# Kernel optimization log

Measured on AMD Instinct MI355X. Metric: run time of the kernel, lower is better.

The kernel has to match this reference:

```python
import jax, jax.numpy as jnp
import numpy as np

C = 128        # in_channels
HEADS = 4
B, D, H, W = 4, 16, 64, 64  # H must equal W for this module's matmul to type-check


def conv1x1(x, Wm, b):
    # 1x1x1 Conv3d == per-voxel linear over channels
    return jnp.einsum('bcdhw,oc->bodhw', x, Wm) + b[None, :, None, None, None]


def setup_inputs() -> dict:
    key = jax.random.key(0)
    ks = jax.random.split(key, 14)
    scale = 1.0 / np.sqrt(C)

    def wmat(k):
        return jax.random.normal(k, (C, C), jnp.float32) * scale

    def bvec(k):
        return jax.random.normal(k, (C,), jnp.float32) * 0.01

    return {
        'x':  jax.random.normal(ks[0], (B, C, D, H, W), jnp.float32),
        'Wq': wmat(ks[1]),  'bq': bvec(ks[2]),
        'Wk': wmat(ks[3]),  'bk': bvec(ks[4]),
        'Wv': wmat(ks[5]),  'bv': bvec(ks[6]),
        'Wa1': wmat(ks[7]), 'ba1': bvec(ks[8]),
        'Wa2': wmat(ks[9]), 'ba2': bvec(ks[10]),
        'Wf': wmat(ks[11]), 'bf': bvec(ks[12]),
    }


def reference(x, Wq, bq, Wk, bk, Wv, bv, Wa1, ba1, Wa2, ba2, Wf, bf):
    b, c, d, h, w = x.shape
    ch = c // HEADS  # channels per head

    q = conv1x1(x, Wq, bq).reshape(b, HEADS, ch, d, h, w)
    k = conv1x1(x, Wk, bk).reshape(b, HEADS, ch, d, h, w)
    v = conv1x1(x, Wv, bv).reshape(b, HEADS, ch, d, h, w)

    # attention over the last spatial axis: (W, H)^T @ (H, W) -> (W, W)
    attn = jnp.einsum('bhcdxi,bhcdxj->bhcdij', q, k)  # [b, heads, ch, d, W, W]
    attn = jax.nn.softmax(attn, axis=-1)
    # (W, W) @ (H=W, W) -> (W, W)
    out = jnp.einsum('bhcdik,bhcdkj->bhcdij', attn, v)
    out = out.reshape(b, c, d, h, w)

    # depth=1 attention layer: conv1x1 -> relu -> conv1x1
    out = conv1x1(jax.nn.relu(conv1x1(out, Wa1, ba1)), Wa2, ba2)
    out = conv1x1(out, Wf, bf)
    return out
```

## Files before the change

kernel.cpp:

```cpp
#include <hip/hip_runtime.h>


#define CCH 128
#define SPB 65536
#define NBATCH 4
#define WTAB 16384

typedef float f32x4 __attribute__((ext_vector_type(4)));
typedef __bf16 bf16x8 __attribute__((ext_vector_type(8)));
typedef short s16x8 __attribute__((ext_vector_type(8)));
typedef unsigned short u16x8 __attribute__((ext_vector_type(8)));
typedef unsigned short u16x4 __attribute__((ext_vector_type(4)));
typedef unsigned int u32x2 __attribute__((ext_vector_type(2)));

template <typename T>
static __device__ __forceinline__ auto mfma_try(T a, T b, f32x4 c, int)
    -> decltype(__builtin_amdgcn_mfma_f32_16x16x32_bf16(a, b, c, 0, 0, 0)) {
  return __builtin_amdgcn_mfma_f32_16x16x32_bf16(a, b, c, 0, 0, 0);
}
template <typename T>
static __device__ __forceinline__ f32x4 mfma_try(T a, T b, f32x4 c, long) {
  return __builtin_amdgcn_mfma_f32_16x16x32_bf16(
      __builtin_bit_cast(bf16x8, a), __builtin_bit_cast(bf16x8, b), c, 0, 0, 0);
}
static __device__ __forceinline__ f32x4 MFMA16(u16x8 a, u16x8 b, f32x4 c) {
  return mfma_try(__builtin_bit_cast(s16x8, a), __builtin_bit_cast(s16x8, b), c, 0);
}

static __device__ __forceinline__ unsigned short f2b(float f) {
  return __builtin_bit_cast(unsigned short, (__bf16)f);
}
static __device__ __forceinline__ unsigned int pk2(float a, float b) {
  return (unsigned int)f2b(a) | ((unsigned int)f2b(b) << 16);
}

static __device__ __forceinline__ void glds16(const unsigned short* g,
                                              unsigned short* l) {
  __builtin_amdgcn_global_load_lds(
      (const __attribute__((address_space(1))) unsigned int*)g,
      (__attribute__((address_space(3))) unsigned int*)l, 16, 0, 0);
}

static __device__ __forceinline__ void bar_lgkm() {
  asm volatile("s_waitcnt lgkmcnt(0)" ::: "memory");
  __builtin_amdgcn_sched_barrier(0);
  __builtin_amdgcn_s_barrier();
  __builtin_amdgcn_sched_barrier(0);
}
static __device__ __forceinline__ void bar_vm0() {
  asm volatile("s_waitcnt vmcnt(0)" ::: "memory");
  __builtin_amdgcn_sched_barrier(0);
  __builtin_amdgcn_s_barrier();
  __builtin_amdgcn_sched_barrier(0);
}

static __device__ __forceinline__ int swzc(int r, int c) {
  int slot = ((c >> 3) ^ (r & 7) ^ ((r >> 3) & 15)) & 15;
  return r * 128 + slot * 8 + (c & 7);
}
static __device__ __forceinline__ int widx(int r, int c) {
  return (r & 64) * 128 + swzc(r & 63, c);
}
static __device__ __forceinline__ int cbix(int o, int s) {
  int slot = ((s >> 3) ^ (o & 15)) & 15;
  return o * 128 + slot * 8 + (s & 7);
}
static __device__ __forceinline__ int swat(int w, int x) {
  int slot = ((x >> 3) ^ (w & 7) ^ ((w >> 3) & 7)) & 7;
  return w * 64 + slot * 8 + (x & 7);
}
static __device__ __forceinline__ int pix(int i, int j) {
  int slot = ((j >> 3) ^ (((i >> 2) & 3) << 1)) & 7;
  return i * 64 + slot * 8 + (j & 7);
}

__global__ __launch_bounds__(256) void prep_w_kernel(
    const float* __restrict__ Wq, const float* __restrict__ Wk,
    const float* __restrict__ Wv, const float* __restrict__ W1,
    const float* __restrict__ W2, const float* __restrict__ W3,
    unsigned short* __restrict__ out)
{
  const float* Ws[6] = {Wq, Wk, Wv, W1, W2, W3};
  const float* W = Ws[blockIdx.x];
  unsigned short* o = out + (size_t)blockIdx.x * WTAB;
  const int tid = threadIdx.x;
#pragma unroll
  for (int p = 0; p < 16; ++p) {
    const int base = p * 1024 + tid * 4;
    const int m = base >> 7;
    const int c0 = base & 127;
    f32x4 v = *(const f32x4*)&W[base];
    u16x4 u;
#pragma unroll
    for (int e = 0; e < 4; ++e) u[e] = f2b(v[e]);
    *(u16x4*)&o[widx(m, c0)] = u;
  }
}

__global__ __launch_bounds__(512, 2) void qkv_kernel(
    const float* __restrict__ X, const unsigned short* __restrict__ Wbf,
    const float* __restrict__ Bq, const float* __restrict__ Bk,
    const float* __restrict__ Bv,
    unsigned short* __restrict__ Yq, unsigned short* __restrict__ Yk,
    unsigned short* __restrict__ Yv)
{
  __shared__ unsigned short wt[3 * WTAB];
  __shared__ unsigned short xb[WTAB];

  const int tid  = threadIdx.x;
  const int wv   = tid >> 6;
  const int lane = tid & 63;
  const int lr   = lane & 15;
  const int lg   = lane >> 4;
  const int sbase = blockIdx.x * 512;
  const size_t xoff = (size_t)blockIdx.y * CCH * SPB;

  const int go = tid * 8;
#pragma unroll
  for (int t = 0; t < 3; ++t)
#pragma unroll
    for (int p = 0; p < 4; ++p)
      glds16(&Wbf[t * WTAB + p * 4096 + go], &wt[t * WTAB + p * 4096 + go]);

  float bq_v[8], bk_v[8], bv_v[8];
#pragma unroll
  for (int of = 0; of < 8; ++of) {
    bq_v[of] = Bq[of * 16 + lr];
    bk_v[of] = Bk[of * 16 + lr];
    bv_v[of] = Bv[of * 16 + lr];
  }

  const int c0  = (tid >> 3) * 2;
  const int sb8 = (tid & 7) * 4;
  const float* xrow = X + xoff + (size_t)c0 * SPB + sbase;
  unsigned int* xb32 = (unsigned int*)xb;

  f32x4 xr[8];
#pragma unroll
  for (int i = 0; i < 4; ++i) {
    xr[i]     = *(const f32x4*)&xrow[sb8 + 32 * i];
    xr[4 + i] = *(const f32x4*)&xrow[SPB + sb8 + 32 * i];
  }
#pragma unroll
  for (int i = 0; i < 4; ++i)
#pragma unroll
    for (int e = 0; e < 4; ++e)
      xb32[swzc(sb8 + 32 * i + e, c0) >> 1] = pk2(xr[i][e], xr[4 + i][e]);
  __syncthreads();

#pragma unroll
  for (int si = 0; si < 4; ++si) {
    const int sg = sbase + si * 128;

    u16x8 afr[4];
#pragma unroll
    for (int ks = 0; ks < 4; ++ks)
      afr[ks] = *(const u16x8*)&xb[swzc(wv * 16 + lr, ks * 32 + lg * 8)];

    if (si < 3) {
      const float* xn = xrow + (si + 1) * 128;
#pragma unroll
      for (int i = 0; i < 4; ++i) {
        xr[i]     = *(const f32x4*)&xn[sb8 + 32 * i];
        xr[4 + i] = *(const f32x4*)&xn[SPB + sb8 + 32 * i];
      }
    }
    bar_lgkm();

    auto conv = [&](int t, const float (&b8)[8], unsigned short* __restrict__ Y) {
      f32x4 acc[8];
#pragma unroll
      for (int of = 0; of < 8; ++of) {
        f32x4 z = {0.f, 0.f, 0.f, 0.f};
        acc[of] = z;
      }
#pragma unroll
      for (int ks = 0; ks < 4; ++ks) {
        const int k0 = ks * 32 + lg * 8;
#pragma unroll
        for (int of = 0; of < 8; ++of) {
          u16x8 wfr = *(const u16x8*)&wt[t * WTAB + widx(of * 16 + lr, k0)];
          acc[of] = MFMA16(afr[ks], wfr, acc[of]);
        }
      }
#pragma unroll
      for (int of = 0; of < 8; ++of) {
        const float b = b8[of];
        u32x2 pk;
        pk.x = pk2(acc[of][0] + b, acc[of][1] + b);
        pk.y = pk2(acc[of][2] + b, acc[of][3] + b);
        *(u32x2*)&xb[cbix(of * 16 + lr, wv * 16 + lg * 4)] = pk;
      }
      bar_lgkm();
#pragma unroll
      for (int p = 0; p < 4; ++p) {
        const int row = p * 32 + (tid >> 4);
        const int sc  = (tid & 15) * 8;
        u16x8 v = *(const u16x8*)&xb[cbix(row, sc)];
        *(u16x8*)&Y[xoff + (size_t)row * SPB + sg + sc] = v;
      }
      bar_lgkm();
    };

    conv(0, bq_v, Yq);
    conv(1, bk_v, Yk);
    conv(2, bv_v, Yv);

    if (si < 3) {
#pragma unroll
      for (int i = 0; i < 4; ++i)
#pragma unroll
        for (int e = 0; e < 4; ++e)
          xb32[swzc(sb8 + 32 * i + e, c0) >> 1] = pk2(xr[i][e], xr[4 + i][e]);
      __syncthreads();
    }
  }
}

__global__ __launch_bounds__(256, 4) void attn64_kernel(
    const unsigned short* __restrict__ Q,
    const unsigned short* __restrict__ K,
    const unsigned short* __restrict__ V,
    unsigned short* __restrict__ O)
{
  __shared__ unsigned short qt[4096];
  __shared__ unsigned short kt[4096];
  __shared__ unsigned short vt[4096];
  __shared__ unsigned short pbuf[4096];

  const int tid  = threadIdx.x;
  const int wv   = tid >> 6;
  const int lane = tid & 63;
  const int lr   = lane & 15;
  const int lg   = lane >> 4;
  const size_t base = (size_t)blockIdx.x * 4096;

  {
    const int x0 = (tid >> 3) * 2;
    const int w0 = (tid & 7) * 8;
    const size_t ga = base + (size_t)x0 * 64 + w0;
    u16x8 qa = *(const u16x8*)&Q[ga], qb = *(const u16x8*)&Q[ga + 64];
    u16x8 ka = *(const u16x8*)&K[ga], kb = *(const u16x8*)&K[ga + 64];
    u16x8 va = *(const u16x8*)&V[ga], vb = *(const u16x8*)&V[ga + 64];
    unsigned int* qt32 = (unsigned int*)qt;
    unsigned int* kt32 = (unsigned int*)kt;
    unsigned int* vt32 = (unsigned int*)vt;
#pragma unroll
    for (int e = 0; e < 8; ++e) {
      const int idx = swat(w0 + e, x0) >> 1;
      qt32[idx] = (unsigned int)qa[e] | ((unsigned int)qb[e] << 16);
      kt32[idx] = (unsigned int)ka[e] | ((unsigned int)kb[e] << 16);
      vt32[idx] = (unsigned int)va[e] | ((unsigned int)vb[e] << 16);
    }
  }
  __syncthreads();

  f32x4 sacc[4];
#pragma unroll
  for (int nf = 0; nf < 4; ++nf) { f32x4 z = {0.f, 0.f, 0.f, 0.f}; sacc[nf] = z; }
#pragma unroll
  for (int ks = 0; ks < 2; ++ks) {
    const int k0 = ks * 32 + lg * 8;
    u16x8 a = *(const u16x8*)&qt[swat(wv * 16 + lr, k0)];
#pragma unroll
    for (int nf = 0; nf < 4; ++nf) {
      u16x8 bb = *(const u16x8*)&kt[swat(nf * 16 + lr, k0)];
      sacc[nf] = MFMA16(a, bb, sacc[nf]);
    }
  }

#pragma unroll
  for (int r = 0; r < 4; ++r) {
    float m = fmaxf(fmaxf(sacc[0][r], sacc[1][r]), fmaxf(sacc[2][r], sacc[3][r]));
    m = fmaxf(m, __shfl_xor(m, 1));
    m = fmaxf(m, __shfl_xor(m, 2));
    m = fmaxf(m, __shfl_xor(m, 4));
    m = fmaxf(m, __shfl_xor(m, 8));
    float sum = 0.f;
#pragma unroll
    for (int nf = 0; nf < 4; ++nf) {
      float p = __expf(sacc[nf][r] - m);
      sacc[nf][r] = p;
      sum += p;
    }
    sum += __shfl_xor(sum, 1);
    sum += __shfl_xor(sum, 2);
    sum += __shfl_xor(sum, 4);
    sum += __shfl_xor(sum, 8);
    const float inv = 1.f / sum;
    const int i = wv * 16 + lg * 4 + r;
#pragma unroll
    for (int nf = 0; nf < 4; ++nf)
      pbuf[pix(i, nf * 16 + lr)] = f2b(sacc[nf][r] * inv);
  }

  f32x4 oacc[4];
#pragma unroll
  for (int nf = 0; nf < 4; ++nf) { f32x4 z = {0.f, 0.f, 0.f, 0.f}; oacc[nf] = z; }
#pragma unroll
  for (int ks = 0; ks < 2; ++ks) {
    const int k0 = ks * 32 + lg * 8;
    u16x8 a = *(const u16x8*)&pbuf[pix(wv * 16 + lr, k0)];
#pragma unroll
    for (int nf = 0; nf < 4; ++nf) {
      u16x8 bb = *(const u16x8*)&vt[swat(nf * 16 + lr, k0)];
      oacc[nf] = MFMA16(bb, a, oacc[nf]);
    }
  }

  {
    const size_t ib = base + (size_t)(16 * wv + lr) * 64 + lg * 4;
#pragma unroll
    for (int nf = 0; nf < 4; ++nf) {
      u32x2 pk;
      pk.x = pk2(oacc[nf][0], oacc[nf][1]);
      pk.y = pk2(oacc[nf][2], oacc[nf][3]);
      *(u32x2*)&O[ib + nf * 16] = pk;
    }
  }
}

__global__ __launch_bounds__(256, 2) void tail_kernel(
    const unsigned short* __restrict__ Xb, const unsigned short* __restrict__ Wbf,
    const float* __restrict__ B1, const float* __restrict__ B2,
    const float* __restrict__ B3, float* __restrict__ OUT)
{
  __shared__ unsigned short wl[16384];
  __shared__ unsigned short xc[16384];
  __shared__ float bias_lds[3][128];

  const int tid  = threadIdx.x;
  const int wv   = tid >> 6;
  const int lane = tid & 63;
  const int lr   = lane & 15;
  const int lg   = lane >> 4;
  const int s0   = blockIdx.x * 128;
  const size_t xbase = (size_t)blockIdx.y * CCH * SPB;
  const int go = tid * 8;

#pragma unroll
  for (int p = 0; p < 8; ++p) glds16(&Wbf[p * 2048 + go], &wl[p * 2048 + go]);

  if (tid < 128) {
    bias_lds[0][tid] = B1[tid];
    bias_lds[1][tid] = B2[tid];
    bias_lds[2][tid] = B3[tid];
  }

  {
    const int cp = tid >> 2;
    const int sq = tid & 3;
    const unsigned short* xa = Xb + xbase + (size_t)(2 * cp) * SPB + s0 + sq * 32;
    const unsigned short* xb = xa + SPB;
    unsigned int* xc32 = (unsigned int*)xc;
#pragma unroll
    for (int i = 0; i < 4; ++i) {
      u16x8 a = *(const u16x8*)&xa[8 * i];
      u16x8 b = *(const u16x8*)&xb[8 * i];
#pragma unroll
      for (int e = 0; e < 8; ++e)
        xc32[swzc(sq * 32 + 8 * i + e, 2 * cp) >> 1] =
            (unsigned int)a[e] | ((unsigned int)b[e] << 16);
    }
  }
  __syncthreads();

  u16x8 bfr[2][4];
#pragma unroll
  for (int nf = 0; nf < 2; ++nf)
#pragma unroll
    for (int ks = 0; ks < 4; ++ks)
      bfr[nf][ks] = *(const u16x8*)&xc[swzc(wv * 32 + nf * 16 + lr, ks * 32 + lg * 8)];

  f32x4 acc[8][2];
  auto gemm_std = [&]() {
#pragma unroll
    for (int mf = 0; mf < 8; ++mf)
#pragma unroll
      for (int nf = 0; nf < 2; ++nf) {
        f32x4 z = {0.f, 0.f, 0.f, 0.f};
        acc[mf][nf] = z;
      }
#pragma unroll
    for (int ks = 0; ks < 4; ++ks) {
      const int k0 = ks * 32 + lg * 8;
#pragma unroll
      for (int mf = 0; mf < 8; ++mf) {
        u16x8 afr = *(const u16x8*)&wl[widx(mf * 16 + lr, k0)];
        acc[mf][0] = MFMA16(afr, bfr[0][ks], acc[mf][0]);
        acc[mf][1] = MFMA16(afr, bfr[1][ks], acc[mf][1]);
      }
    }
  };

  auto epi_chain = [&](int ci, bool relu) {
#pragma unroll
    for (int mf = 0; mf < 8; ++mf)
#pragma unroll
      for (int nf = 0; nf < 2; ++nf) {
        const int s = wv * 32 + nf * 16 + lr;
        const int c0 = mf * 16 + lg * 4;
        f32x4 bb = *(const f32x4*)&bias_lds[ci][c0];
        float v0 = acc[mf][nf][0] + bb[0];
        float v1 = acc[mf][nf][1] + bb[1];
        float v2 = acc[mf][nf][2] + bb[2];
        float v3 = acc[mf][nf][3] + bb[3];
        if (relu) {
          v0 = fmaxf(v0, 0.f); v1 = fmaxf(v1, 0.f);
          v2 = fmaxf(v2, 0.f); v3 = fmaxf(v3, 0.f);
        }
        u32x2 pk;
        pk.x = pk2(v0, v1);
        pk.y = pk2(v2, v3);
        *(u32x2*)&xc[swzc(s, c0)] = pk;
      }
#pragma unroll
    for (int nf = 0; nf < 2; ++nf)
#pragma unroll
      for (int ks = 0; ks < 4; ++ks)
        bfr[nf][ks] = *(const u16x8*)&xc[swzc(wv * 32 + nf * 16 + lr, ks * 32 + lg * 8)];
  };

#pragma unroll
  for (int j = 0; j < 2; ++j) {
    gemm_std();
    bar_lgkm();
    const unsigned short* Wn = Wbf + (size_t)(j + 1) * WTAB;
#pragma unroll
    for (int p = 0; p < 8; ++p) glds16(&Wn[p * 2048 + go], &wl[p * 2048 + go]);
    epi_chain(j, j == 0);
    bar_vm0();
  }

  {
    f32x4 acc3[2][8];
#pragma unroll
    for (int sf = 0; sf < 2; ++sf)
#pragma unroll
      for (int of = 0; of < 8; ++of) {
        f32x4 z = {0.f, 0.f, 0.f, 0.f};
        acc3[sf][of] = z;
      }
#pragma unroll
    for (int ks = 0; ks < 4; ++ks) {
      const int k0 = ks * 32 + lg * 8;
#pragma unroll
      for (int of = 0; of < 8; ++of) {
        u16x8 wfr = *(const u16x8*)&wl[widx(of * 16 + lr, k0)];
        acc3[0][of] = MFMA16(bfr[0][ks], wfr, acc3[0][of]);
        acc3[1][of] = MFMA16(bfr[1][ks], wfr, acc3[1][of]);
      }
    }
    const int sb = s0 + wv * 32 + lg * 4;
#pragma unroll
    for (int sf = 0; sf < 2; ++sf)
#pragma unroll
      for (int of = 0; of < 8; ++of) {
        const float b = bias_lds[2][of * 16 + lr];
        f32x4 v = acc3[sf][of];
        v[0] += b; v[1] += b; v[2] += b; v[3] += b;
        *(f32x4*)&OUT[xbase + (size_t)(of * 16 + lr) * SPB + sb + sf * 16] = v;
      }
  }
}

extern "C" void kernel_launch(void* const* d_in, const int* in_sizes, int n_in,
                              void* d_out, int out_size, void* d_ws, size_t ws_size,
                              hipStream_t stream) {
  const float* x   = (const float*)d_in[0];
  const float* Wq  = (const float*)d_in[1];  const float* bq  = (const float*)d_in[2];
  const float* Wk  = (const float*)d_in[3];  const float* bk  = (const float*)d_in[4];
  const float* Wv  = (const float*)d_in[5];  const float* bv  = (const float*)d_in[6];
  const float* Wa1 = (const float*)d_in[7];  const float* ba1 = (const float*)d_in[8];
  const float* Wa2 = (const float*)d_in[9];  const float* ba2 = (const float*)d_in[10];
  const float* Wf  = (const float*)d_in[11]; const float* bf_ = (const float*)d_in[12];

  unsigned short* qb  = (unsigned short*)d_ws;
  unsigned short* wbf = qb + (size_t)NBATCH * CCH * SPB;
  unsigned short* kb = (unsigned short*)d_out;
  unsigned short* vb = kb + (size_t)NBATCH * CCH * SPB;

  prep_w_kernel<<<6, 256, 0, stream>>>(Wq, Wk, Wv, Wa1, Wa2, Wf, wbf);

  qkv_kernel<<<dim3(SPB / 512, NBATCH), 512, 0, stream>>>(
      x, wbf, bq, bk, bv, qb, kb, vb);

  attn64_kernel<<<NBATCH * CCH * 16, 256, 0, stream>>>(qb, kb, vb, qb);

  tail_kernel<<<dim3(SPB / 128, NBATCH), 256, 0, stream>>>(
      qb, wbf + (size_t)3 * WTAB, ba1, ba2, bf_, (float*)d_out);
}
```

Baseline: 177.3 us.

## Stream QKV weights through one LDS buffer and swizzle block order

The QKV kernel now keeps a single 32 KB weight tile in LDS instead of all three. It streams the next projection's weights with async global-to-LDS loads that overlap the epilogue and stores, and moves the biases into LDS. Together these cut LDS use and registers so launch bounds can allow four blocks per CU. All three kernels also remap block indices with an XCD-style swizzle, so neighbouring spatial tiles land on the same chiplet for cache locality. The cost is one extra weight load per projection per sub-tile, plus added barrier and vmcnt synchronisation complexity.

Measured after the change: 295.0 us. 1.66x slower.

```diff
diff --git a/kernel.cpp b/kernel.cpp
--- a/kernel.cpp
+++ b/kernel.cpp
@@ -49,6 +49,12 @@
 }
 static __device__ __forceinline__ void bar_vm0() {
   asm volatile("s_waitcnt vmcnt(0)" ::: "memory");
+  __builtin_amdgcn_sched_barrier(0);
+  __builtin_amdgcn_s_barrier();
+  __builtin_amdgcn_sched_barrier(0);
+}
+static __device__ __forceinline__ void bar_vm4_lgkm() {
+  asm volatile("s_waitcnt vmcnt(4) lgkmcnt(0)" ::: "memory");
   __builtin_amdgcn_sched_barrier(0);
   __builtin_amdgcn_s_barrier();
   __builtin_amdgcn_sched_barrier(0);
@@ -97,37 +103,35 @@
   }
 }
 
-__global__ __launch_bounds__(512, 2) void qkv_kernel(
+__global__ __launch_bounds__(512, 4) void qkv_kernel(
     const float* __restrict__ X, const unsigned short* __restrict__ Wbf,
     const float* __restrict__ Bq, const float* __restrict__ Bk,
     const float* __restrict__ Bv,
     unsigned short* __restrict__ Yq, unsigned short* __restrict__ Yk,
     unsigned short* __restrict__ Yv)
 {
-  __shared__ unsigned short wt[3 * WTAB];
+  __shared__ unsigned short wt[WTAB];
   __shared__ unsigned short xb[WTAB];
+  __shared__ float bias_lds[3][128];
 
   const int tid  = threadIdx.x;
   const int wv   = tid >> 6;
   const int lane = tid & 63;
   const int lr   = lane & 15;
   const int lg   = lane >> 4;
-  const int sbase = blockIdx.x * 512;
-  const size_t xoff = (size_t)blockIdx.y * CCH * SPB;
-
+  const int lin  = blockIdx.x;
+  const int swz  = ((lin & 7) << 6) | (lin >> 3);
+  const int sbase = (swz & 127) * 512;
+  const size_t xoff = (size_t)(swz >> 7) * CCH * SPB;
   const int go = tid * 8;
-#pragma unroll
-  for (int t = 0; t < 3; ++t)
-#pragma unroll
-    for (int p = 0; p < 4; ++p)
-      glds16(&Wbf[t * WTAB + p * 4096 + go], &wt[t * WTAB + p * 4096 + go]);
-
-  float bq_v[8], bk_v[8], bv_v[8];
-#pragma unroll
-  for (int of = 0; of < 8; ++of) {
-    bq_v[of] = Bq[of * 16 + lr];
-    bk_v[of] = Bk[of * 16 + lr];
-    bv_v[of] = Bv[of * 16 + lr];
+
+#pragma unroll
+  for (int p = 0; p < 4; ++p) glds16(&Wbf[p * 4096 + go], &wt[p * 4096 + go]);
+
+  if (tid < 128) {
+    bias_lds[0][tid] = Bq[tid];
+    bias_lds[1][tid] = Bk[tid];
+    bias_lds[2][tid] = Bv[tid];
   }
 
   const int c0  = (tid >> 3) * 2;
@@ -167,7 +171,8 @@
     }
     bar_lgkm();
 
-    auto conv = [&](int t, const float (&b8)[8], unsigned short* __restrict__ Y) {
+    auto conv = [&](int ci, const unsigned short* Wnext,
+                    unsigned short* __restrict__ Y, bool last) {
       f32x4 acc[8];
 #pragma unroll
       for (int of = 0; of < 8; ++of) {
@@ -179,13 +184,19 @@
         const int k0 = ks * 32 + lg * 8;
 #pragma unroll
         for (int of = 0; of < 8; ++of) {
-          u16x8 wfr = *(const u16x8*)&wt[t * WTAB + widx(of * 16 + lr, k0)];
+          u16x8 wfr = *(const u16x8*)&wt[widx(of * 16 + lr, k0)];
           acc[of] = MFMA16(afr[ks], wfr, acc[of]);
         }
       }
+      bar_lgkm();
+      if (Wnext) {
+#pragma unroll
+        for (int p = 0; p < 4; ++p)
+          glds16(&Wnext[p * 4096 + go], &wt[p * 4096 + go]);
+      }
 #pragma unroll
       for (int of = 0; of < 8; ++of) {
-        const float b = b8[of];
+        const float b = bias_lds[ci][of * 16 + lr];
         u32x2 pk;
         pk.x = pk2(acc[of][0] + b, acc[of][1] + b);
         pk.y = pk2(acc[of][2] + b, acc[of][3] + b);
@@ -199,12 +210,12 @@
         u16x8 v = *(const u16x8*)&xb[cbix(row, sc)];
         *(u16x8*)&Y[xoff + (size_t)row * SPB + sg + sc] = v;
       }
-      bar_lgkm();
+      if (!last) bar_vm4_lgkm();
     };
 
-    conv(0, bq_v, Yq);
-    conv(1, bk_v, Yk);
-    conv(2, bv_v, Yv);
+    conv(0, Wbf + WTAB,     Yq, false);
+    conv(1, Wbf + 2 * WTAB, Yk, false);
+    conv(2, si < 3 ? Wbf : nullptr, Yv, si == 3);
 
     if (si < 3) {
 #pragma unroll
@@ -212,7 +223,7 @@
 #pragma unroll
         for (int e = 0; e < 4; ++e)
           xb32[swzc(sb8 + 32 * i + e, c0) >> 1] = pk2(xr[i][e], xr[4 + i][e]);
-      __syncthreads();
+      bar_lgkm();
     }
   }
 }
@@ -233,7 +244,9 @@
   const int lane = tid & 63;
   const int lr   = lane & 15;
   const int lg   = lane >> 4;
-  const size_t base = (size_t)blockIdx.x * 4096;
+  const int bid  = blockIdx.x;
+  const int bs   = ((bid & 7) << 10) | (bid >> 3);
+  const size_t base = (size_t)bs * 4096;
 
   {
     const int x0 = (tid >> 3) * 2;
@@ -334,7 +347,9 @@
   const int lane = tid & 63;
   const int lr   = lane & 15;
   const int lg   = lane >> 4;
-  const int s0   = blockIdx.x * 128;
+  const int bx   = blockIdx.x;
+  const int bxs  = ((bx & 7) << 6) | (bx >> 3);
+  const int s0   = bxs * 128;
   const size_t xbase = (size_t)blockIdx.y * CCH * SPB;
   const int go = tid * 8;
 
@@ -399,8 +414,8 @@
 #pragma unroll
       for (int nf = 0; nf < 2; ++nf) {
         const int s = wv * 32 + nf * 16 + lr;
-        const int c0 = mf * 16 + lg * 4;
-        f32x4 bb = *(const f32x4*)&bias_lds[ci][c0];
+        const int cc = mf * 16 + lg * 4;
+        f32x4 bb = *(const f32x4*)&bias_lds[ci][cc];
         float v0 = acc[mf][nf][0] + bb[0];
         float v1 = acc[mf][nf][1] + bb[1];
         float v2 = acc[mf][nf][2] + bb[2];
@@ -412,7 +427,7 @@
         u32x2 pk;
         pk.x = pk2(v0, v1);
         pk.y = pk2(v2, v3);
-        *(u32x2*)&xc[swzc(s, c0)] = pk;
+        *(u32x2*)&xc[swzc(s, cc)] = pk;
       }
 #pragma unroll
     for (int nf = 0; nf < 2; ++nf)
@@ -482,8 +497,7 @@
 
   prep_w_kernel<<<6, 256, 0, stream>>>(Wq, Wk, Wv, Wa1, Wa2, Wf, wbf);
 
-  qkv_kernel<<<dim3(SPB / 512, NBATCH), 512, 0, stream>>>(
-      x, wbf, bq, bk, bv, qb, kb, vb);
+  qkv_kernel<<<512, 512, 0, stream>>>(x, wbf, bq, bk, bv, qb, kb, vb);
 
   attn64_kernel<<<NBATCH * CCH * 16, 256, 0, stream>>>(qb, kb, vb, qb);
 
```
